# Kernel optimization log

Hardware: AMD Instinct MI355X
Metric: run time of the kernel (lower is better)

## Reference

```python
import jax, jax.numpy as jnp
import numpy as np

DECAY = 0.99
EPS = 1e-5
COMMIT = 0.25

def setup_inputs() -> dict:
    key = jax.random.key(0)
    k1, k2 = jax.random.split(key)
    inputs = jax.random.normal(k1, (2, 64, 48, 48, 48), dtype=jnp.float32)
    emb_weight = jax.random.normal(k2, (256, 64), dtype=jnp.float32)
    return {
        "inputs": inputs,
        "emb_weight": emb_weight,
        "ema_cluster_size": jnp.zeros((256,), jnp.float32),
        "ema_w": emb_weight.copy(),  # registered buffer initialized as clone of embedding
    }

def reference(inputs, emb_weight, ema_cluster_size, ema_w):
    B, C, D, H, W = inputs.shape
    K = emb_weight.shape[0]
    # quantize: channel-last flatten [B*D*H*W, C]
    flat_input = jnp.transpose(inputs, (0, 2, 3, 4, 1)).reshape(-1, C)
    # pairwise squared distances via norms + matmul
    distances = ((flat_input ** 2).sum(axis=1, keepdims=True)
                 + (emb_weight ** 2).sum(axis=1)[None, :]
                 - 2.0 * flat_input @ emb_weight.T)  # [N, K]
    encoding_indices = jnp.argmin(distances, axis=1)  # [N]
    # embed: gather codebook rows, reshape to channel-first [B, C, D, H, W]
    quantized = jnp.transpose(emb_weight[encoding_indices].reshape(B, D, H, W, C), (0, 4, 1, 2, 3))
    # EMA codebook update (training branch; one-hot sums expressed as segment reductions)
    encodings_sum = jax.ops.segment_sum(jnp.ones(flat_input.shape[0], jnp.float32), encoding_indices, num_segments=K)
    dw = jax.ops.segment_sum(flat_input, encoding_indices, num_segments=K)  # [K, C]
    new_cluster_size = DECAY * ema_cluster_size + (1.0 - DECAY) * encodings_sum
    n = new_cluster_size.sum()
    weights = (new_cluster_size + EPS) / (n + K * EPS) * n
    new_ema_w = DECAY * ema_w + (1.0 - DECAY) * dw
    new_emb_weight = new_ema_w / weights[:, None]
    # commitment loss (quantized detached) scaled by 10, straight-through estimator
    loss = COMMIT * jnp.mean((jax.lax.stop_gradient(quantized) - inputs) ** 2) * 10.0
    quantized_out = inputs + jax.lax.stop_gradient(quantized - inputs)
    enc_idx = encoding_indices.reshape(B, D, H, W)
    return (quantized_out, loss, enc_idx, encodings_sum, new_emb_weight)
```

## Files before the change

### kernel.cpp

```cpp
#include <hip/hip_runtime.h>
#include <hip/hip_bf16.h>

#define SPA 110592
#define NPOS 221184
#define NELEM 14155776
#define KCODES 256
#define CCH 64
#define DWBLK 432
#define DWTHR 512
#define EPS_TIE 0.0625f

typedef __attribute__((ext_vector_type(8))) short bf16x8;
typedef __attribute__((ext_vector_type(16))) float f32x16;

__device__ __forceinline__ void bf16split(float v, short& h, short& l) {
    unsigned bits = __builtin_bit_cast(unsigned, v);
    h = (short)(bits >> 16);
    float hf = __builtin_bit_cast(float, bits & 0xFFFF0000u);
    float res = v - hf;
    l = (short)(__builtin_bit_cast(unsigned, res) >> 16);
}

__global__ __launch_bounds__(256) void vq_init(
    const float* __restrict__ emb, float* __restrict__ en2,
    float* __restrict__ dw, float* __restrict__ hist, float* __restrict__ loss)
{
    int t = blockIdx.x * 256 + threadIdx.x;
    if (t < CCH * KCODES) dw[t] = 0.f;
    if (t < KCODES) {
        const float* e = emb + (t << 6);
        float s = 0.f;
#pragma unroll
        for (int c = 0; c < CCH; ++c) s = fmaf(e[c], e[c], s);
        en2[t] = s;
        hist[t] = 0.f;
    }
    if (t == 0) loss[0] = 0.f;
}

__global__ __launch_bounds__(256, 2) void vq_argmin_mfma(
    const float* __restrict__ in, const float* __restrict__ emb,
    const float* __restrict__ en2, float* __restrict__ qout,
    float* __restrict__ encout, float* __restrict__ hist,
    float* __restrict__ loss)
{
    __shared__ __align__(16) short xh[8][128][8];
    __shared__ __align__(16) short xl[8][128][8];
    __shared__ float e2s[KCODES];
    __shared__ float pm1[4][128], pm2[4][128];
    __shared__ int   pk1[4][128], pk2[4][128];
    __shared__ int   bestkS[128];
    __shared__ float lhist[KCODES];
    __shared__ float lred[4];

    int tid  = threadIdx.x;
    int w    = tid >> 6, lane = tid & 63;
    int hi   = lane >> 5, col = lane & 31;
    int wbase = w * 64;

    int blk = blockIdx.x;
    int b   = (blk >= 864) ? 1 : 0;
    int s0  = (blk - b * 864) * 128;
    const float* xbase = in + b * (CCH * SPA) + s0;

    if (tid < KCODES) { e2s[tid] = en2[tid]; lhist[tid] = 0.f; }

    bf16x8 Ah[2][4], Al[2][4];
#pragma unroll
    for (int ct = 0; ct < 2; ++ct) {
        int code = wbase + ct * 32 + col;
        const float* er = emb + (code << 6) + hi * 8;
#pragma unroll
        for (int j = 0; j < 4; ++j) {
            bf16x8 hfr, lfr;
#pragma unroll
            for (int jj = 0; jj < 8; ++jj) {
                short hs, ls; bf16split(er[j * 16 + jj], hs, ls);
                hfr[jj] = hs; lfr[jj] = ls;
            }
            Ah[ct][j] = hfr; Al[ct][j] = lfr;
        }
    }

    {
        int tg = tid >> 7, p = tid & 127;
        const float* xb = xbase + p;
#pragma unroll
        for (int cb = 0; cb < 4; ++cb) {
            int c0 = tg * 32 + cb * 8;
            bf16x8 hfr, lfr;
#pragma unroll
            for (int jj = 0; jj < 8; ++jj) {
                short hs, ls; bf16split(xb[(c0 + jj) * SPA], hs, ls);
                hfr[jj] = hs; lfr[jj] = ls;
            }
            *(bf16x8*)&xh[c0 >> 3][p][0] = hfr;
            *(bf16x8*)&xl[c0 >> 3][p][0] = lfr;
        }
    }
    __syncthreads();

#pragma unroll 1
    for (int pt = 0; pt < 4; ++pt) {
        int pos = pt * 32 + col;
        f32x16 c0, c1;
#pragma unroll
        for (int i = 0; i < 16; ++i) { c0[i] = 0.f; c1[i] = 0.f; }

#pragma unroll
        for (int j = 0; j < 4; ++j) {
            bf16x8 bh = *(const bf16x8*)&xh[j * 2 + hi][pos][0];
            bf16x8 bl = *(const bf16x8*)&xl[j * 2 + hi][pos][0];
            c0 = __builtin_amdgcn_mfma_f32_32x32x16_bf16(Ah[0][j], bh, c0, 0, 0, 0);
            c1 = __builtin_amdgcn_mfma_f32_32x32x16_bf16(Ah[1][j], bh, c1, 0, 0, 0);
            c0 = __builtin_amdgcn_mfma_f32_32x32x16_bf16(Ah[0][j], bl, c0, 0, 0, 0);
            c1 = __builtin_amdgcn_mfma_f32_32x32x16_bf16(Ah[1][j], bl, c1, 0, 0, 0);
            c0 = __builtin_amdgcn_mfma_f32_32x32x16_bf16(Al[0][j], bh, c0, 0, 0, 0);
            c1 = __builtin_amdgcn_mfma_f32_32x32x16_bf16(Al[1][j], bh, c1, 0, 0, 0);
        }

        float m1 = 1e30f, m2 = 1e30f; int k1 = 0, k2 = 0;
#pragma unroll
        for (int ct = 0; ct < 2; ++ct) {
#pragma unroll
            for (int r = 0; r < 16; ++r) {
                int kc  = wbase + ct * 32 + (r & 3) + 8 * (r >> 2) + 4 * hi;
                float d = fmaf(-2.f, (ct ? c1[r] : c0[r]), e2s[kc]);
                bool lt1 = d < m1, lt2 = d < m2;
                float nm2 = lt1 ? m1 : (lt2 ? d : m2);
                int   nk2 = lt1 ? k1 : (lt2 ? kc : k2);
                m1 = lt1 ? d : m1; k1 = lt1 ? kc : k1;
                m2 = nm2; k2 = nk2;
            }
        }
        float om1 = __shfl_xor(m1, 32, 64), om2 = __shfl_xor(m2, 32, 64);
        int   ok1 = __shfl_xor(k1, 32, 64), ok2 = __shfl_xor(k2, 32, 64);
        if (om1 < m1) {
            float t2 = (m1 < om2) ? m1 : om2;
            int   tk = (m1 < om2) ? k1 : ok2;
            m2 = t2; k2 = tk; m1 = om1; k1 = ok1;
        } else {
            float t2 = (om1 < m2) ? om1 : m2;
            int   tk = (om1 < m2) ? ok1 : k2;
            m2 = t2; k2 = tk;
        }
        if (hi == 0) {
            pm1[w][pos] = m1; pk1[w][pos] = k1;
            pm2[w][pos] = m2; pk2[w][pos] = k2;
        }
    }
    __syncthreads();

    if (tid < 128) {
        int p = tid;
        float M1 = pm1[0][p], M2 = pm2[0][p];
        int   K1 = pk1[0][p], K2 = pk2[0][p];
#pragma unroll
        for (int ww = 1; ww < 4; ++ww) {
            float om1 = pm1[ww][p], om2 = pm2[ww][p];
            int   ok1 = pk1[ww][p], ok2 = pk2[ww][p];
            if (om1 < M1) {
                float t2 = (M1 < om2) ? M1 : om2;
                int   tk = (M1 < om2) ? K1 : ok2;
                M2 = t2; K2 = tk; M1 = om1; K1 = ok1;
            } else {
                float t2 = (om1 < M2) ? om1 : M2;
                int   tk = (om1 < M2) ? ok1 : K2;
                M2 = t2; K2 = tk;
            }
        }
        int bk = K1;
        if (M2 <= M1 + EPS_TIE) {
            int ka = min(K1, K2), kb = max(K1, K2);
            const float* xb2 = xbase + p;
            const float* ea  = emb + (ka << 6);
            const float* eb2 = emb + (kb << 6);
            float x2 = 0.f, da = 0.f, db = 0.f;
#pragma unroll 4
            for (int c = 0; c < CCH; ++c) {
                float xv = xb2[c * SPA];
                x2 = fmaf(xv, xv, x2);
                da = fmaf(xv, ea[c], da);
                db = fmaf(xv, eb2[c], db);
            }
            float Da = x2 + en2[ka] - 2.f * da;
            float Db = x2 + en2[kb] - 2.f * db;
            bk = (Db < Da) ? kb : ka;
        }
        bestkS[p] = bk;
        encout[b * SPA + s0 + p] = (float)bk;
        atomicAdd(&lhist[bk], 1.0f);
    }
    __syncthreads();

    {
        int tg = tid >> 7, p = tid & 127;
        int k = bestkS[p];
        const float* ee  = emb + (k << 6) + tg * 32;
        const float* xb3 = xbase + p;
        float* qp = qout + b * (CCH * SPA) + s0 + p;
        float lsum = 0.f;
#pragma unroll
        for (int c = 0; c < 32; ++c) {
            float q  = ee[c];
            float xv = xb3[(tg * 32 + c) * SPA];
            float d  = q - xv;
            lsum = fmaf(d, d, lsum);
            qp[(tg * 32 + c) * SPA] = q;
        }
        for (int off = 32; off > 0; off >>= 1) lsum += __shfl_down(lsum, off, 64);
        if (lane == 0) lred[w] = lsum;
    }
    __syncthreads();
    if (tid == 0)
        unsafeAtomicAdd(loss, (lred[0] + lred[1] + lred[2] + lred[3]) * (2.5f / 14155776.f));
    if (tid < KCODES && lhist[tid] != 0.f)
        unsafeAtomicAdd(&hist[tid], lhist[tid]);
}

__global__ __launch_bounds__(DWTHR) void vq_dw_part(
    const float* __restrict__ in, const float* __restrict__ encout,
    float* __restrict__ partial)
{
    __shared__ float l[CCH * KCODES];
    int tid = threadIdx.x;
    for (int i = tid; i < CCH * KCODES; i += DWTHR) l[i] = 0.f;
    __syncthreads();

    int n = blockIdx.x * DWTHR + tid;
    int b = (n >= SPA) ? 1 : 0;
    int s = n - b * SPA;
    int k = (int)encout[n];
    const float* xp = in + b * (CCH * SPA) + s;
#pragma unroll
    for (int c = 0; c < CCH; ++c)
        atomicAdd(&l[(c << 8) + (k ^ (c & 31))], xp[c * SPA]);
    __syncthreads();

    float* pp = partial + (size_t)blockIdx.x * (CCH * KCODES);
    for (int i = tid; i < CCH * KCODES; i += DWTHR) {
        int k2 = i >> 6, c = i & 63;
        pp[i] = l[(c << 8) + (k2 ^ (c & 31))];
    }
}

__global__ __launch_bounds__(256) void vq_dw_reduce(
    const float* __restrict__ partial, float* __restrict__ dw)
{
    __shared__ float acc[4][64];
    int t = threadIdx.x, lane6 = t & 63, tsub = t >> 6;
    int i = blockIdx.x * 64 + lane6;
    float s = 0.f;
    for (int p = tsub * 108; p < tsub * 108 + 108; ++p)
        s += partial[(size_t)p * (CCH * KCODES) + i];
    acc[tsub][lane6] = s;
    __syncthreads();
    if (tsub == 0)
        dw[i] = (acc[0][lane6] + acc[1][lane6]) + (acc[2][lane6] + acc[3][lane6]);
}

__global__ __launch_bounds__(DWTHR) void vq_dw_atomic(
    const float* __restrict__ in, const float* __restrict__ encout,
    float* __restrict__ dw)
{
    __shared__ float l[CCH * KCODES];
    int tid = threadIdx.x;
    for (int i = tid; i < CCH * KCODES; i += DWTHR) l[i] = 0.f;
    __syncthreads();
    int n = blockIdx.x * DWTHR + tid;
    int b = (n >= SPA) ? 1 : 0;
    int s = n - b * SPA;
    int k = (int)encout[n];
    const float* xp = in + b * (CCH * SPA) + s;
#pragma unroll
    for (int c = 0; c < CCH; ++c)
        atomicAdd(&l[(c << 8) + (k ^ (c & 31))], xp[c * SPA]);
    __syncthreads();
    for (int i = tid; i < CCH * KCODES; i += DWTHR) {
        int k2 = i >> 6, c = i & 63;
        unsafeAtomicAdd(&dw[i], l[(c << 8) + (k2 ^ (c & 31))]);
    }
}

__global__ __launch_bounds__(256) void vq_ema_w(
    const float* __restrict__ csize, const float* __restrict__ hist,
    float* __restrict__ wbuf)
{
    __shared__ float red[KCODES];
    int t = threadIdx.x;
    float ncs = 0.99f * csize[t] + 0.01f * hist[t];
    red[t] = ncs;
    __syncthreads();
    for (int off = 128; off > 0; off >>= 1) {
        if (t < off) red[t] += red[t + off];
        __syncthreads();
    }
    float nsum = red[0];
    wbuf[t] = (ncs + 1e-5f) / (nsum + 256.f * 1e-5f) * nsum;
}

__global__ __launch_bounds__(256) void vq_emb(
    const float* __restrict__ emaw, const float* __restrict__ dw,
    const float* __restrict__ wbuf, float* __restrict__ embo)
{
    int i = blockIdx.x * 256 + threadIdx.x;
    float nw = fmaf(0.01f, dw[i], 0.99f * emaw[i]);
    embo[i] = nw / wbuf[i >> 6];
}

extern "C" void kernel_launch(void* const* d_in, const int* in_sizes, int n_in,
                              void* d_out, int out_size, void* d_ws, size_t ws_size,
                              hipStream_t stream)
{
    const float* in   = (const float*)d_in[0];
    const float* emb  = (const float*)d_in[1];
    const float* cs   = (const float*)d_in[2];
    const float* emaw = (const float*)d_in[3];

    float* out  = (float*)d_out;
    float* qout = out;
    float* loss = out + NELEM;
    float* enc  = loss + 1;
    float* hist = enc + NPOS;
    float* embo = hist + KCODES;

    float* en2     = (float*)d_ws;
    float* wbuf    = en2 + KCODES;
    float* dw      = wbuf + KCODES;
    float* partial = dw + CCH * KCODES;

    size_t need = (size_t)(2 * KCODES + CCH * KCODES) * 4
                + (size_t)DWBLK * CCH * KCODES * 4;
    bool use_part = (ws_size >= need);

    vq_init<<<dim3(64), dim3(256), 0, stream>>>(emb, en2, dw, hist, loss);
    vq_argmin_mfma<<<dim3(1728), dim3(256), 0, stream>>>(in, emb, en2, qout, enc, hist, loss);
    if (use_part) {
        vq_dw_part<<<dim3(DWBLK), dim3(DWTHR), 0, stream>>>(in, enc, partial);
        vq_dw_reduce<<<dim3(256), dim3(256), 0, stream>>>(partial, dw);
    } else {
        vq_dw_atomic<<<dim3(DWBLK), dim3(DWTHR), 0, stream>>>(in, enc, dw);
    }
    vq_ema_w<<<dim3(1), dim3(256), 0, stream>>>(cs, hist, wbuf);
    vq_emb<<<dim3(64), dim3(256), 0, stream>>>(emaw, dw, wbuf, embo);
}
```

Measured before the change: 268.1 us.

## Pack code index into distance bits, reuse LDS input, raise occupancy, rebalance dw partials

The argmin top-2 tracking now stores the code index in the low mantissa bits of each distance and uses fminf/fmaxf merges, which removes the separate index registers and shared arrays. Launch bounds rise to 4 blocks per CU. The loss and quantize pass rebuilds x from the bf16 hi/lo pairs already in LDS instead of reloading it from global memory, and the tie-break drops the x² term it does not need. The dw partial pass moves to 512 blocks of 432 positions each, with a matching reduce. Risks: the packed index costs a little distance precision, the bf16 hi+lo rebuild is not exact, and the partial buffer in the workspace gets larger.

```diff
diff --git a/kernel.cpp b/kernel.cpp
--- a/kernel.cpp
+++ b/kernel.cpp
@@ -6,6 +6,8 @@
 #define NELEM 14155776
 #define KCODES 256
 #define CCH 64
+#define PBLK 512
+#define PPOS 432
 #define DWBLK 432
 #define DWTHR 512
 #define EPS_TIE 0.0625f
@@ -21,6 +23,27 @@
     l = (short)(__builtin_bit_cast(unsigned, res) >> 16);
 }
 
+__device__ __forceinline__ float bf16join(short h, short l) {
+    float hf = __builtin_bit_cast(float, ((unsigned)(unsigned short)h) << 16);
+    float lf = __builtin_bit_cast(float, ((unsigned)(unsigned short)l) << 16);
+    return hf + lf;
+}
+
+__device__ __forceinline__ float dpack(float d, int k) {
+    unsigned bits = (__builtin_bit_cast(unsigned, d) & 0xFFFFFF00u) | (unsigned)k;
+    return __builtin_bit_cast(float, bits);
+}
+__device__ __forceinline__ int dkey(float d) {
+    return (int)(__builtin_bit_cast(unsigned, d) & 0xFFu);
+}
+
+__device__ __forceinline__ void top2merge(float& m1, float& m2, float o1, float o2) {
+    float a = fminf(m1, o1);
+    float b = fmaxf(m1, o1);
+    m2 = fminf(b, fminf(m2, o2));
+    m1 = a;
+}
+
 __global__ __launch_bounds__(256) void vq_init(
     const float* __restrict__ emb, float* __restrict__ en2,
     float* __restrict__ dw, float* __restrict__ hist, float* __restrict__ loss)
@@ -38,7 +61,7 @@
     if (t == 0) loss[0] = 0.f;
 }
 
-__global__ __launch_bounds__(256, 2) void vq_argmin_mfma(
+__global__ __launch_bounds__(256, 4) void vq_argmin_mfma(
     const float* __restrict__ in, const float* __restrict__ emb,
     const float* __restrict__ en2, float* __restrict__ qout,
     float* __restrict__ encout, float* __restrict__ hist,
@@ -48,7 +71,6 @@
     __shared__ __align__(16) short xl[8][128][8];
     __shared__ float e2s[KCODES];
     __shared__ float pm1[4][128], pm2[4][128];
-    __shared__ int   pk1[4][128], pk2[4][128];
     __shared__ int   bestkS[128];
     __shared__ float lhist[KCODES];
     __shared__ float lred[4];
@@ -119,72 +141,46 @@
             c1 = __builtin_amdgcn_mfma_f32_32x32x16_bf16(Al[1][j], bh, c1, 0, 0, 0);
         }
 
-        float m1 = 1e30f, m2 = 1e30f; int k1 = 0, k2 = 0;
+        float m1 = 1e30f, m2 = 1e30f;
 #pragma unroll
         for (int ct = 0; ct < 2; ++ct) {
 #pragma unroll
             for (int r = 0; r < 16; ++r) {
                 int kc  = wbase + ct * 32 + (r & 3) + 8 * (r >> 2) + 4 * hi;
-                float d = fmaf(-2.f, (ct ? c1[r] : c0[r]), e2s[kc]);
-                bool lt1 = d < m1, lt2 = d < m2;
-                float nm2 = lt1 ? m1 : (lt2 ? d : m2);
-                int   nk2 = lt1 ? k1 : (lt2 ? kc : k2);
-                m1 = lt1 ? d : m1; k1 = lt1 ? kc : k1;
-                m2 = nm2; k2 = nk2;
-            }
-        }
-        float om1 = __shfl_xor(m1, 32, 64), om2 = __shfl_xor(m2, 32, 64);
-        int   ok1 = __shfl_xor(k1, 32, 64), ok2 = __shfl_xor(k2, 32, 64);
-        if (om1 < m1) {
-            float t2 = (m1 < om2) ? m1 : om2;
-            int   tk = (m1 < om2) ? k1 : ok2;
-            m2 = t2; k2 = tk; m1 = om1; k1 = ok1;
-        } else {
-            float t2 = (om1 < m2) ? om1 : m2;
-            int   tk = (om1 < m2) ? ok1 : k2;
-            m2 = t2; k2 = tk;
-        }
-        if (hi == 0) {
-            pm1[w][pos] = m1; pk1[w][pos] = k1;
-            pm2[w][pos] = m2; pk2[w][pos] = k2;
-        }
+                float d = dpack(fmaf(-2.f, (ct ? c1[r] : c0[r]), e2s[kc]), kc);
+                float lo  = fminf(d, m1);
+                float hi2 = fmaxf(d, m1);
+                m2 = fminf(hi2, m2);
+                m1 = lo;
+            }
+        }
+        top2merge(m1, m2, __shfl_xor(m1, 32, 64), __shfl_xor(m2, 32, 64));
+        if (hi == 0) { pm1[w][pos] = m1; pm2[w][pos] = m2; }
     }
     __syncthreads();
 
     if (tid < 128) {
         int p = tid;
         float M1 = pm1[0][p], M2 = pm2[0][p];
-        int   K1 = pk1[0][p], K2 = pk2[0][p];
-#pragma unroll
-        for (int ww = 1; ww < 4; ++ww) {
-            float om1 = pm1[ww][p], om2 = pm2[ww][p];
-            int   ok1 = pk1[ww][p], ok2 = pk2[ww][p];
-            if (om1 < M1) {
-                float t2 = (M1 < om2) ? M1 : om2;
-                int   tk = (M1 < om2) ? K1 : ok2;
-                M2 = t2; K2 = tk; M1 = om1; K1 = ok1;
-            } else {
-                float t2 = (om1 < M2) ? om1 : M2;
-                int   tk = (om1 < M2) ? ok1 : K2;
-                M2 = t2; K2 = tk;
-            }
-        }
+#pragma unroll
+        for (int ww = 1; ww < 4; ++ww)
+            top2merge(M1, M2, pm1[ww][p], pm2[ww][p]);
+        int K1 = dkey(M1), K2 = dkey(M2);
         int bk = K1;
         if (M2 <= M1 + EPS_TIE) {
             int ka = min(K1, K2), kb = max(K1, K2);
             const float* xb2 = xbase + p;
             const float* ea  = emb + (ka << 6);
             const float* eb2 = emb + (kb << 6);
-            float x2 = 0.f, da = 0.f, db = 0.f;
+            float da = 0.f, db = 0.f;
 #pragma unroll 4
             for (int c = 0; c < CCH; ++c) {
                 float xv = xb2[c * SPA];
-                x2 = fmaf(xv, xv, x2);
                 da = fmaf(xv, ea[c], da);
                 db = fmaf(xv, eb2[c], db);
             }
-            float Da = x2 + en2[ka] - 2.f * da;
-            float Db = x2 + en2[kb] - 2.f * db;
+            float Da = e2s[ka] - 2.f * da;
+            float Db = e2s[kb] - 2.f * db;
             bk = (Db < Da) ? kb : ka;
         }
         bestkS[p] = bk;
@@ -196,17 +192,22 @@
     {
         int tg = tid >> 7, p = tid & 127;
         int k = bestkS[p];
-        const float* ee  = emb + (k << 6) + tg * 32;
-        const float* xb3 = xbase + p;
+        const float* ee = emb + (k << 6) + tg * 32;
         float* qp = qout + b * (CCH * SPA) + s0 + p;
         float lsum = 0.f;
 #pragma unroll
-        for (int c = 0; c < 32; ++c) {
-            float q  = ee[c];
-            float xv = xb3[(tg * 32 + c) * SPA];
-            float d  = q - xv;
-            lsum = fmaf(d, d, lsum);
-            qp[(tg * 32 + c) * SPA] = q;
+        for (int cb = 0; cb < 4; ++cb) {
+            int oct = tg * 4 + cb;
+            bf16x8 hfr = *(const bf16x8*)&xh[oct][p][0];
+            bf16x8 lfr = *(const bf16x8*)&xl[oct][p][0];
+#pragma unroll
+            for (int jj = 0; jj < 8; ++jj) {
+                float xv = bf16join(hfr[jj], lfr[jj]);
+                float q  = ee[cb * 8 + jj];
+                float d  = q - xv;
+                lsum = fmaf(d, d, lsum);
+                qp[(tg * 32 + cb * 8 + jj) * SPA] = q;
+            }
         }
         for (int off = 32; off > 0; off >>= 1) lsum += __shfl_down(lsum, off, 64);
         if (lane == 0) lred[w] = lsum;
@@ -218,27 +219,31 @@
         unsafeAtomicAdd(&hist[tid], lhist[tid]);
 }
 
-__global__ __launch_bounds__(DWTHR) void vq_dw_part(
+__global__ __launch_bounds__(512) void vq_dw_part(
     const float* __restrict__ in, const float* __restrict__ encout,
     float* __restrict__ partial)
 {
     __shared__ float l[CCH * KCODES];
     int tid = threadIdx.x;
-    for (int i = tid; i < CCH * KCODES; i += DWTHR) l[i] = 0.f;
-    __syncthreads();
-
-    int n = blockIdx.x * DWTHR + tid;
-    int b = (n >= SPA) ? 1 : 0;
-    int s = n - b * SPA;
-    int k = (int)encout[n];
-    const float* xp = in + b * (CCH * SPA) + s;
-#pragma unroll
-    for (int c = 0; c < CCH; ++c)
-        atomicAdd(&l[(c << 8) + (k ^ (c & 31))], xp[c * SPA]);
+#pragma unroll
+    for (int i = tid; i < CCH * KCODES; i += 512) l[i] = 0.f;
+    __syncthreads();
+
+    if (tid < PPOS) {
+        int n = blockIdx.x * PPOS + tid;
+        int b = (n >= SPA) ? 1 : 0;
+        int s = n - b * SPA;
+        int k = (int)encout[n];
+        const float* xp = in + b * (CCH * SPA) + s;
+#pragma unroll
+        for (int c = 0; c < CCH; ++c)
+            atomicAdd(&l[(c << 8) + (k ^ (c & 31))], xp[c * SPA]);
+    }
     __syncthreads();
 
     float* pp = partial + (size_t)blockIdx.x * (CCH * KCODES);
-    for (int i = tid; i < CCH * KCODES; i += DWTHR) {
+#pragma unroll
+    for (int i = tid; i < CCH * KCODES; i += 512) {
         int k2 = i >> 6, c = i & 63;
         pp[i] = l[(c << 8) + (k2 ^ (c & 31))];
     }
@@ -251,7 +256,7 @@
     int t = threadIdx.x, lane6 = t & 63, tsub = t >> 6;
     int i = blockIdx.x * 64 + lane6;
     float s = 0.f;
-    for (int p = tsub * 108; p < tsub * 108 + 108; ++p)
+    for (int p = tsub * 128; p < tsub * 128 + 128; ++p)
         s += partial[(size_t)p * (CCH * KCODES) + i];
     acc[tsub][lane6] = s;
     __syncthreads();
@@ -330,13 +335,13 @@
     float* partial = dw + CCH * KCODES;
 
     size_t need = (size_t)(2 * KCODES + CCH * KCODES) * 4
-                + (size_t)DWBLK * CCH * KCODES * 4;
+                + (size_t)PBLK * CCH * KCODES * 4;
     bool use_part = (ws_size >= need);
 
     vq_init<<<dim3(64), dim3(256), 0, stream>>>(emb, en2, dw, hist, loss);
     vq_argmin_mfma<<<dim3(1728), dim3(256), 0, stream>>>(in, emb, en2, qout, enc, hist, loss);
     if (use_part) {
-        vq_dw_part<<<dim3(DWBLK), dim3(DWTHR), 0, stream>>>(in, enc, partial);
+        vq_dw_part<<<dim3(PBLK), dim3(512), 0, stream>>>(in, enc, partial);
         vq_dw_reduce<<<dim3(256), dim3(256), 0, stream>>>(partial, dw);
     } else {
         vq_dw_atomic<<<dim3(DWBLK), dim3(DWTHR), 0, stream>>>(in, enc, dw);
```

Result: slower. 275.8 us (+2.9%).
